# Kernel tuning notes

Hardware: AMD Instinct MI355X
Metric: run time of the kernel (lower is better)

Reference implementation:

```python
import jax, jax.numpy as jnp
import numpy as np
from jax import lax

D, H, HD, DEPTH = 200, 10, 20, 12   # embed_dim, heads, head_dim, depth
NCH, A = 64, 8                       # EEG channels x time windows -> 512 patches (+cls)
NUM_REL = (2 * NCH - 1) * (2 * A - 1) + 3  # 1908


def make_rel_index(wh, ww):
    # exact port of the torch relative_position_index construction
    coords = np.stack(np.meshgrid(np.arange(wh), np.arange(ww), indexing='ij')).reshape(2, -1)
    rel = (coords[:, :, None] - coords[:, None, :]).transpose(1, 2, 0)
    rel[..., 0] += wh - 1
    rel[..., 1] += ww - 1
    rel[..., 0] *= 2 * ww - 1
    n = wh * ww + 1
    num_rel = (2 * wh - 1) * (2 * ww - 1) + 3
    idx = np.zeros((n, n), dtype=np.int32)
    idx[1:, 1:] = rel.sum(-1)
    idx[0, :] = num_rel - 3
    idx[:, 0] = num_rel - 2
    idx[0, 0] = num_rel - 1
    return idx


def gelu(x):
    return jax.nn.gelu(x, approximate=False)


def layer_norm(x, g, b, eps=1e-6):
    m = x.mean(-1, keepdims=True)
    v = ((x - m) ** 2).mean(-1, keepdims=True)
    return (x - m) * lax.rsqrt(v + eps) * g + b


def group_norm(x, g, b, groups=4, eps=1e-5):
    B, C, Hh, W = x.shape
    xr = x.reshape(B, groups, C // groups, Hh, W)
    m = xr.mean((2, 3, 4), keepdims=True)
    v = ((xr - m) ** 2).mean((2, 3, 4), keepdims=True)
    xr = ((xr - m) * lax.rsqrt(v + eps)).reshape(B, C, Hh, W)
    return xr * g[None, :, None, None] + b[None, :, None, None]


def conv2d(x, w, b, stride, pad):
    y = lax.conv_general_dilated(x, w, window_strides=stride, padding=pad,
                                 dimension_numbers=('NCHW', 'OIHW', 'NCHW'))
    return y + b[None, :, None, None]


def setup_inputs() -> dict:
    B = 8
    key = jax.random.key(0)
    ks = iter(jax.random.split(key, 40))
    rn = lambda shape, s=0.02: jax.random.normal(next(ks), shape, dtype=jnp.float32) * s
    z = lambda shape: jnp.zeros(shape, jnp.float32)
    o = lambda shape: jnp.ones(shape, jnp.float32)
    inp = {}
    inp['x'] = jax.random.normal(next(ks), (B, NCH, A, 200), dtype=jnp.float32)
    inp['conv1_w'] = rn((8, 1, 1, 15), 0.1); inp['conv1_b'] = z(8)
    inp['gn1_g'] = o(8); inp['gn1_b'] = z(8)
    inp['conv2_w'] = rn((8, 8, 1, 3), 0.1); inp['conv2_b'] = z(8)
    inp['gn2_g'] = o(8); inp['gn2_b'] = z(8)
    inp['conv3_w'] = rn((8, 8, 1, 3), 0.1); inp['conv3_b'] = z(8)
    inp['gn3_g'] = o(8); inp['gn3_b'] = z(8)
    inp['cls_token'] = rn((1, 1, D)); inp['pos_embed'] = rn((1, NCH + 1, D))
    inp['time_embed'] = rn((1, 16, D))
    inp['ln1_g'] = o((DEPTH, D)); inp['ln1_b'] = z((DEPTH, D))
    inp['qkv_w'] = rn((DEPTH, 3 * D, D))
    inp['rel_bias_table'] = rn((DEPTH, NUM_REL, H))
    inp['proj_w'] = rn((DEPTH, D, D)); inp['proj_b'] = z((DEPTH, D))
    inp['gamma1'] = 0.1 * o((DEPTH, D))
    inp['ln2_g'] = o((DEPTH, D)); inp['ln2_b'] = z((DEPTH, D))
    inp['fc1_w'] = rn((DEPTH, 4 * D, D)); inp['fc1_b'] = z((DEPTH, 4 * D))
    inp['fc2_w'] = rn((DEPTH, D, 4 * D)); inp['fc2_b'] = z((DEPTH, D))
    inp['gamma2'] = 0.1 * o((DEPTH, D))
    inp['fc_norm_g'] = o(D); inp['fc_norm_b'] = z(D)
    inp['head_w'] = rn((4, D)); inp['head_b'] = z(4)
    inp['rel_pos_index'] = jnp.asarray(make_rel_index(NCH, A))
    return inp


def reference(x, conv1_w, conv1_b, gn1_g, gn1_b, conv2_w, conv2_b, gn2_g, gn2_b,
              conv3_w, conv3_b, gn3_g, gn3_b, cls_token, pos_embed, time_embed,
              ln1_g, ln1_b, qkv_w, rel_bias_table, proj_w, proj_b, gamma1,
              ln2_g, ln2_b, fc1_w, fc1_b, fc2_w, fc2_b, gamma2,
              fc_norm_g, fc_norm_b, head_w, head_b, rel_pos_index):
    B = x.shape[0]
    # TemporalConv patch embed: (B, NCH, A, 200) -> (B, NCH*A, D)
    h = x.reshape(B, 1, NCH * A, -1)
    h = gelu(group_norm(conv2d(h, conv1_w, conv1_b, (1, 8), [(0, 0), (7, 7)]), gn1_g, gn1_b))
    h = gelu(group_norm(conv2d(h, conv2_w, conv2_b, (1, 1), [(0, 0), (1, 1)]), gn2_g, gn2_b))
    h = gelu(group_norm(conv2d(h, conv3_w, conv3_b, (1, 1), [(0, 0), (1, 1)]), gn3_g, gn3_b))
    h = h.transpose(0, 2, 3, 1).reshape(B, NCH * A, D)  # 'B C NA T -> B NA (T C)'
    # cls token + per-electrode pos embed + temporal embed
    h = jnp.concatenate([jnp.broadcast_to(cls_token, (B, 1, D)), h], axis=1)
    pos_p = jnp.repeat(pos_embed[:, 1:, None, :], A, axis=2).reshape(1, NCH * A, D)
    h = h + jnp.concatenate([pos_embed[:, :1], pos_p], axis=1)
    te = jnp.broadcast_to(time_embed[:, None, :A, :], (1, NCH, A, D)).reshape(1, NCH * A, D)
    h = jnp.concatenate([h[:, :1], h[:, 1:] + te], axis=1)
    N = h.shape[1]  # 513
    scale = HD ** -0.5
    for d in range(DEPTH):
        y = layer_norm(h, ln1_g[d], ln1_b[d])
        qkv = (y @ qkv_w[d].T).reshape(B, N, 3, H, HD).transpose(2, 0, 3, 1, 4)
        q, k, v = qkv[0], qkv[1], qkv[2]
        attn = jnp.einsum('bhnd,bhmd->bhnm', q * scale, k)
        attn = attn + rel_bias_table[d][rel_pos_index].transpose(2, 0, 1)[None]
        attn = jax.nn.softmax(attn, axis=-1)
        o = jnp.einsum('bhnm,bhmd->bhnd', attn, v)
        o = o.transpose(0, 2, 1, 3).reshape(B, N, D) @ proj_w[d].T + proj_b[d]
        h = h + gamma1[d] * o
        y = layer_norm(h, ln2_g[d], ln2_b[d])
        y = gelu(y @ fc1_w[d].T + fc1_b[d]) @ fc2_w[d].T + fc2_b[d]
        h = h + gamma2[d] * y
    pooled = layer_norm(h[:, 1:].mean(1), fc_norm_g, fc_norm_b)  # use_mean_pooling
    return pooled @ head_w.T + head_b
```

## Files before the change

kernel.cpp:

```cpp
#include <hip/hip_runtime.h>
#include <math.h>

#define DEV static __device__ __forceinline__

typedef __attribute__((ext_vector_type(8))) short bf16x8;
typedef __attribute__((ext_vector_type(4))) float f32x4;

DEV float gelu_exact(float x) {
    return 0.5f * x * (1.0f + erff(x * 0.70710678118654752f));
}

DEV short f2bf(float f) {
    union { float f; unsigned u; } v; v.f = f;
    unsigned r = v.u + 0x7FFF + ((v.u >> 16) & 1);
    return (short)(r >> 16);
}

DEV float bf2f(unsigned short b) {
    union { unsigned u; float f; } v; v.u = ((unsigned)b) << 16;
    return v.f;
}

DEV unsigned pack2bf(float a, float b) {
    return ((unsigned)(unsigned short)f2bf(a)) | (((unsigned)(unsigned short)f2bf(b)) << 16);
}

DEV void gload_lds16(const void* g, void* lds) {
    __builtin_amdgcn_global_load_lds(
        (const __attribute__((address_space(1))) void*)g,
        (__attribute__((address_space(3))) void*)lds, 16, 0, 0);
}

__global__ void conv1_kernel(const float* __restrict__ x, const float* __restrict__ w,
                             const float* __restrict__ bias, float* __restrict__ out) {
    int idx = blockIdx.x * blockDim.x + threadIdx.x;
    const int total = 8 * 8 * 512 * 25;
    if (idx >= total) return;
    int ow = idx % 25;
    int p  = (idx / 25) % 512;
    int oc = (idx / (25 * 512)) % 8;
    int b  = idx / (25 * 512 * 8);
    const float* xp = x + b * 512 * 200 + p * 200;
    const float* wp = w + oc * 15;
    float acc = bias[oc];
    int t0 = ow * 8 - 7;
#pragma unroll
    for (int k = 0; k < 15; k++) {
        int t = t0 + k;
        if (t >= 0 && t < 200) acc += wp[k] * xp[t];
    }
    out[idx] = acc;
}

__global__ void conv3x1_kernel(const float* __restrict__ in, const float* __restrict__ w,
                               const float* __restrict__ bias, float* __restrict__ out) {
    int idx = blockIdx.x * blockDim.x + threadIdx.x;
    const int total = 8 * 8 * 512 * 25;
    if (idx >= total) return;
    int ow = idx % 25;
    int p  = (idx / 25) % 512;
    int oc = (idx / 12800) & 7;
    int b  = idx / 102400;
    float acc = bias[oc];
#pragma unroll
    for (int ic = 0; ic < 8; ic++) {
        const float* ip = in + b * 102400 + ic * 12800 + p * 25;
        const float* wp = w + oc * 24 + ic * 3;
        if (ow > 0)  acc += wp[0] * ip[ow - 1];
        acc += wp[1] * ip[ow];
        if (ow < 24) acc += wp[2] * ip[ow + 1];
    }
    out[idx] = acc;
}

__global__ void gn_stats_kernel(const float* __restrict__ buf, float* __restrict__ stats) {
    int b = blockIdx.x >> 2, g = blockIdx.x & 3;
    const float* base = buf + b * 102400 + g * 2 * 12800;
    float s = 0.f, s2 = 0.f;
    for (int l = threadIdx.x; l < 25600; l += 256) {
        float v = base[l];
        s += v; s2 += v * v;
    }
    __shared__ float ss[256], ss2[256];
    ss[threadIdx.x] = s; ss2[threadIdx.x] = s2;
    __syncthreads();
    for (int o = 128; o; o >>= 1) {
        if (threadIdx.x < o) { ss[threadIdx.x] += ss[threadIdx.x + o]; ss2[threadIdx.x] += ss2[threadIdx.x + o]; }
        __syncthreads();
    }
    if (threadIdx.x == 0) {
        float m = ss[0] / 25600.f;
        float v = ss2[0] / 25600.f - m * m;
        stats[blockIdx.x * 2] = m;
        stats[blockIdx.x * 2 + 1] = v;
    }
}

__global__ void gn_apply_kernel(float* __restrict__ buf, const float* __restrict__ stats,
                                const float* __restrict__ g, const float* __restrict__ bb) {
    int idx = blockIdx.x * blockDim.x + threadIdx.x;
    if (idx >= 8 * 102400) return;
    int c = (idx / 12800) & 7;
    int b = idx / 102400;
    int grp = c >> 1;
    float m = stats[(b * 4 + grp) * 2];
    float v = stats[(b * 4 + grp) * 2 + 1];
    float val = (buf[idx] - m) * rsqrtf(v + 1e-5f) * g[c] + bb[c];
    buf[idx] = gelu_exact(val);
}

__global__ void embed_kernel(const float* __restrict__ conv, const float* __restrict__ cls,
                             const float* __restrict__ pos, const float* __restrict__ te,
                             float* __restrict__ h) {
    int idx = blockIdx.x * blockDim.x + threadIdx.x;
    if (idx >= 8 * 513 * 200) return;
    int d = idx % 200;
    int n = (idx / 200) % 513;
    int b = idx / (200 * 513);
    float val;
    if (n == 0) {
        val = cls[d] + pos[d];
    } else {
        int p = n - 1;
        int t = d >> 3;
        int c = d & 7;
        val = conv[b * 102400 + c * 12800 + p * 25 + t];
        int ch = p >> 3, tw = p & 7;
        val += pos[(1 + ch) * 200 + d] + te[tw * 200 + d];
    }
    h[idx] = val;
}

__global__ void convpad_kernel(const float* __restrict__ src, short* __restrict__ dst,
                               int R, int K, int KP) {
    int idx = blockIdx.x * blockDim.x + threadIdx.x;
    if (idx >= R * KP) return;
    int r = idx / KP, c = idx % KP;
    dst[idx] = (c < K) ? f2bf(src[r * K + c]) : (short)0;
}

__global__ __launch_bounds__(256) void bias_lds_kernel(const float* __restrict__ table,
                                                       const int* __restrict__ ridx,
                                                       short* __restrict__ bias) {
    __shared__ float tl[1908];
    const int qt = blockIdx.x, hh = blockIdx.y, d = blockIdx.z;
    const float* tab = table + d * 19080;
    for (int i = threadIdx.x; i < 1908; i += 256) tl[i] = tab[i * 10 + hh];
    __syncthreads();
    const int q0 = qt * 64;
    const int nrows = min(64, 513 - q0);
    short* obase = bias + ((size_t)d * 10 + hh) * 513 * 576;
#pragma unroll 2
    for (int lin = threadIdx.x; lin < nrows * 144; lin += 256) {
        int r = lin / 144, j = lin % 144;
        int q = q0 + r;
        const int* rp = ridx + q * 513;
        int k0 = j * 4;
        float v[4];
#pragma unroll
        for (int e = 0; e < 4; e++) {
            int k = k0 + e;
            v[e] = (k < 513) ? tl[rp[k]] : 0.f;
        }
        uint2 pk;
        pk.x = pack2bf(v[0], v[1]);
        pk.y = pack2bf(v[2], v[3]);
        *(uint2*)&obase[(size_t)q * 576 + k0] = pk;
    }
}

__global__ __launch_bounds__(256) void ln_kernel(const float* __restrict__ in,
                                                 const float* __restrict__ g,
                                                 const float* __restrict__ b,
                                                 short* __restrict__ out) {
    int row = blockIdx.x * 4 + (threadIdx.x >> 6);
    int lane = threadIdx.x & 63;
    const float* x = in + (size_t)row * 200;
    float v[4];
    float s = 0.f;
#pragma unroll
    for (int i = 0; i < 4; i++) {
        int d = lane + i * 64;
        v[i] = (d < 200) ? x[d] : 0.f;
        s += v[i];
    }
#pragma unroll
    for (int o = 32; o; o >>= 1) s += __shfl_xor(s, o);
    float mean = s * (1.f / 200.f);
    float s2 = 0.f;
#pragma unroll
    for (int i = 0; i < 4; i++) {
        int d = lane + i * 64;
        float dv = (d < 200) ? (v[i] - mean) : 0.f;
        s2 += dv * dv;
    }
#pragma unroll
    for (int o = 32; o; o >>= 1) s2 += __shfl_xor(s2, o);
    float rstd = rsqrtf(s2 * (1.f / 200.f) + 1e-6f);
#pragma unroll
    for (int i = 0; i < 4; i++) {
        int d = lane + i * 64;
        float val = (d < 200) ? (v[i] - mean) * rstd * g[d] + b[d] : 0.f;
        out[(size_t)row * 256 + d] = f2bf(val);
    }
}

template <int EPI, int BM, int BN>
__global__ __launch_bounds__(256) void gemm_bf(const short* __restrict__ A,
                                               const short* __restrict__ W,
                                               float* __restrict__ Cf,
                                               short* __restrict__ Cb,
                                               const float* __restrict__ res,
                                               const float* __restrict__ bias,
                                               const float* __restrict__ gamma,
                                               int M, int N, int KP, int ldc, int NPout,
                                               short* __restrict__ Qb = nullptr,
                                               short* __restrict__ Kb = nullptr,
                                               short* __restrict__ Vt = nullptr) {
    constexpr int WM = BM / 2, WN = BN / 2;
    constexpr int AM = WM / 16, BNr = WN / 16;
    constexpr int LOADS = (BM + BN) / 32;
    __shared__ __align__(16) short Ss[2][(BM + BN) * 64];

    const int tid = threadIdx.x;
    const int w = tid >> 6, l = tid & 63;
    const int wm = (w >> 1) * WM, wn = (w & 1) * WN;
    const int bm = blockIdx.y * BM, bn = blockIdx.x * BN;

    f32x4 acc[AM][BNr] = {};

    auto stage = [&](int buf, int k0) {
#pragma unroll
        for (int it = 0; it < LOADS; it++) {
            int lin = it * 256 + tid;
            int row = lin >> 3, slot = lin & 7;
            int srcslot = slot ^ (row & 7);
            const short* g;
            if (it * 32 < BM) {
                g = A + (size_t)(bm + row) * KP + k0 + srcslot * 8;
            } else {
                g = W + (size_t)(bn + row - BM) * KP + k0 + srcslot * 8;
            }
            gload_lds16(g, (char*)Ss[buf] + lin * 16);
        }
    };

    const int nk = KP >> 6;
    stage(0, 0);
    int cur = 0;
    for (int kstep = 0; kstep < nk; kstep++) {
        if (kstep + 1 < nk) {
            stage(cur ^ 1, (kstep + 1) << 6);
            if constexpr (LOADS == 6) asm volatile("s_waitcnt vmcnt(6)" ::: "memory");
            else                      asm volatile("s_waitcnt vmcnt(4)" ::: "memory");
        } else {
            asm volatile("s_waitcnt vmcnt(0)" ::: "memory");
        }
        __builtin_amdgcn_s_barrier();

        const char* Sc = (const char*)Ss[cur];
#pragma unroll
        for (int kk = 0; kk < 2; kk++) {
            const int kbyte = kk * 64 + (l >> 4) * 16;
            bf16x8 af[AM], bfr[BNr];
#pragma unroll
            for (int i = 0; i < AM; i++) {
                int r = wm + i * 16 + (l & 15);
                af[i] = *(const bf16x8*)(Sc + r * 128 + (kbyte ^ ((r & 7) << 4)));
            }
#pragma unroll
            for (int j = 0; j < BNr; j++) {
                int r = BM + wn + j * 16 + (l & 15);
                bfr[j] = *(const bf16x8*)(Sc + r * 128 + (kbyte ^ ((r & 7) << 4)));
            }
#pragma unroll
            for (int i = 0; i < AM; i++)
#pragma unroll
                for (int j = 0; j < BNr; j++)
                    acc[i][j] = __builtin_amdgcn_mfma_f32_16x16x32_bf16(af[i], bfr[j], acc[i][j], 0, 0, 0);
        }
        __builtin_amdgcn_s_barrier();
        cur ^= 1;
    }

    const int col0 = bn + wn + (l & 15);
    const int rbase = (l >> 4) * 4;
#pragma unroll
    for (int i = 0; i < AM; i++) {
#pragma unroll
        for (int r = 0; r < 4; r++) {
            int gm = bm + wm + i * 16 + rbase + r;
            if (gm >= M) continue;
#pragma unroll
            for (int j = 0; j < BNr; j++) {
                int gn = col0 + j * 16;
                float v = acc[i][j][r];
                if (EPI == 0) {
                    if (gn < N) Cf[(size_t)gm * ldc + gn] = v;
                } else if (EPI == 1) {
                    if (gn < N) Cf[(size_t)gm * ldc + gn] =
                        res[(size_t)gm * ldc + gn] + gamma[gn] * (v + bias[gn]);
                } else if (EPI == 2) {
                    if (gn < NPout)
                        Cb[(size_t)gm * ldc + gn] = (gn < N) ? f2bf(gelu_exact(v + bias[gn])) : (short)0;
                } else {
                    if (gn < 600) {
                        int bb2 = gm / 513, n = gm - bb2 * 513;
                        if (gn < 200) {
                            int hq = gn / 20, dq = gn - hq * 20;
                            Qb[((size_t)(bb2 * 10 + hq) * 576 + n) * 32 + dq] =
                                f2bf(v * 0.22360679774997896f);
                        } else if (gn < 400) {
                            int gk = gn - 200, hk = gk / 20, dk = gk - hk * 20;
                            Kb[((size_t)(bb2 * 10 + hk) * 576 + n) * 32 + dk] = f2bf(v);
                        } else {
                            int gv = gn - 400, hv = gv / 20, dv2 = gv - hv * 20;
                            Vt[((size_t)(bb2 * 10 + hv) * 32 + dv2) * 576 + n] = f2bf(v);
                        }
                    }
                }
            }
        }
    }
}

__global__ __launch_bounds__(256) void attn_mfma2(const short* __restrict__ Qb,
                                                  const short* __restrict__ Kb,
                                                  const short* __restrict__ Vt,
                                                  const short* __restrict__ biasb,
                                                  short* __restrict__ ob) {
    __shared__ __align__(16) short Klds[2][64 * 32];
    __shared__ __align__(16) short Vlds[2][32 * 64];
    __shared__ __align__(16) short Blds[2][64 * 64];
    __shared__ __align__(16) short Pl[4 * 16 * 72];

    const int orig = blockIdx.x;
    const int wg = (orig & 7) * 90 + (orig >> 3);
    const int hh = wg / 72;
    const int rem = wg % 72;
    const int qt = rem >> 3, b = rem & 7;

    const int t = threadIdx.x, wave = t >> 6, l = t & 63;
    const int lq = l & 15, hi = l >> 4;
    const int n = qt * 64 + wave * 16 + lq;
    const int nc = min(n, 512);

    const size_t bh = (size_t)(b * 10 + hh);
    const short* Kbase = Kb + bh * 576 * 32;
    const short* Vbase = Vt + bh * 32 * 576;
    const short* Bbase = biasb + (size_t)hh * 513 * 576;

    bf16x8 qf = *(const bf16x8*)&Qb[(bh * 576 + nc) * 32 + hi * 8];

    const int krow = t >> 2, kch = t & 3;
    const short* ksrc = Kbase + (size_t)krow * 32 + (kch ^ ((krow >> 2) & 3)) * 8;
    const int vrow = t >> 3, vch = t & 7;
    const short* vsrc = Vbase + (size_t)vrow * 576 + (vch ^ (vrow & 7)) * 8;
    const int b0row = t >> 3, b0ch = t & 7;
    const short* bsrc0 = Bbase + (size_t)min(qt * 64 + b0row, 512) * 576 + (b0ch ^ (b0row & 7)) * 8;
    const int b1row = 32 + (t >> 3);
    const short* bsrc1 = Bbase + (size_t)min(qt * 64 + b1row, 512) * 576 + (b0ch ^ (b1row & 7)) * 8;

    float mrun = -1e30f, lsum = 0.f;
    f32x4 oacc0 = {}, oacc1 = {};
    const f32x4 zero4 = {};

    gload_lds16(ksrc, (char*)Klds[0] + t * 16);
    gload_lds16(vsrc, (char*)Vlds[0] + t * 16);
    gload_lds16(bsrc0, (char*)Blds[0] + t * 16);
    gload_lds16(bsrc1, (char*)Blds[0] + 4096 + t * 16);

    int cur = 0;
    for (int kt = 0; kt < 9; kt++) {
        const int koff = kt * 64;
        if (kt < 8) {
            const int knext = koff + 64;
            gload_lds16(ksrc + (size_t)knext * 32, (char*)Klds[cur ^ 1] + t * 16);
            gload_lds16(vsrc + knext, (char*)Vlds[cur ^ 1] + t * 16);
            gload_lds16(bsrc0 + knext, (char*)Blds[cur ^ 1] + t * 16);
            gload_lds16(bsrc1 + knext, (char*)Blds[cur ^ 1] + 4096 + t * 16);
            asm volatile("s_waitcnt vmcnt(4)" ::: "memory");
        } else {
            asm volatile("s_waitcnt vmcnt(0)" ::: "memory");
        }
        __builtin_amdgcn_s_barrier();

        const short* Kc = Klds[cur];
        const short* Vc = Vlds[cur];
        const short* Bc = Blds[cur];

        f32x4 s[4];
        __builtin_amdgcn_s_setprio(1);
#pragma unroll
        for (int c = 0; c < 4; c++) {
            int r = c * 16 + lq;
            bf16x8 kf = *(const bf16x8*)((const char*)Kc + r * 64 + ((hi ^ ((lq >> 2) & 3)) << 4));
            s[c] = __builtin_amdgcn_mfma_f32_16x16x32_bf16(kf, qf, zero4, 0, 0, 0);
        }
        __builtin_amdgcn_s_setprio(0);

        const int brow = wave * 16 + lq;
        float sv[4][4];
        float tm = -1e30f;
#pragma unroll
        for (int c = 0; c < 4; c++) {
            uint2 bl = *(const uint2*)((const char*)Bc + brow * 128 +
                                       (((2 * c + (hi >> 1)) ^ (lq & 7)) << 4) + (hi & 1) * 8);
            float bv[4] = { bf2f((unsigned short)(bl.x & 0xFFFF)), bf2f((unsigned short)(bl.x >> 16)),
                            bf2f((unsigned short)(bl.y & 0xFFFF)), bf2f((unsigned short)(bl.y >> 16)) };
            int kglob = koff + c * 16 + hi * 4;
#pragma unroll
            for (int r = 0; r < 4; r++) {
                float val = s[c][r] + bv[r];
                if (kglob + r > 512) val = -1e30f;
                sv[c][r] = val;
                tm = fmaxf(tm, val);
            }
        }
        tm = fmaxf(tm, __shfl_xor(tm, 16));
        tm = fmaxf(tm, __shfl_xor(tm, 32));
        float mnew = fmaxf(mrun, tm);
        float resc = __expf(mrun - mnew);
        mrun = mnew;

        float ts = 0.f;
#pragma unroll
        for (int c = 0; c < 4; c++) {
            float p0 = __expf(sv[c][0] - mnew);
            float p1 = __expf(sv[c][1] - mnew);
            float p2 = __expf(sv[c][2] - mnew);
            float p3 = __expf(sv[c][3] - mnew);
            ts += (p0 + p1) + (p2 + p3);
            uint2 pk;
            pk.x = pack2bf(p0, p1);
            pk.y = pack2bf(p2, p3);
            *(uint2*)&Pl[wave * 1152 + lq * 72 + c * 16 + hi * 4] = pk;
        }
        ts += __shfl_xor(ts, 16);
        ts += __shfl_xor(ts, 32);
        lsum = lsum * resc + ts;
        oacc0 *= resc;
        oacc1 *= resc;

        __builtin_amdgcn_s_setprio(1);
#pragma unroll
        for (int kc = 0; kc < 2; kc++) {
            bf16x8 pf = *(const bf16x8*)&Pl[wave * 1152 + lq * 72 + kc * 32 + hi * 8];
            bf16x8 vf0 = *(const bf16x8*)((const char*)Vc + lq * 128 +
                                          (((kc * 4 + hi) ^ (lq & 7)) << 4));
            bf16x8 vf1 = *(const bf16x8*)((const char*)Vc + (16 + lq) * 128 +
                                          (((kc * 4 + hi) ^ (lq & 7)) << 4));
            oacc0 = __builtin_amdgcn_mfma_f32_16x16x32_bf16(vf0, pf, oacc0, 0, 0, 0);
            oacc1 = __builtin_amdgcn_mfma_f32_16x16x32_bf16(vf1, pf, oacc1, 0, 0, 0);
        }
        __builtin_amdgcn_s_setprio(0);

        __builtin_amdgcn_s_barrier();
        cur ^= 1;
    }

    if (n < 513) {
        float inv = 1.f / lsum;
        short* op = ob + (size_t)(b * 513 + n) * 256 + hh * 20;
        {
            uint2 pk;
            pk.x = pack2bf(oacc0[0] * inv, oacc0[1] * inv);
            pk.y = pack2bf(oacc0[2] * inv, oacc0[3] * inv);
            *(uint2*)&op[hi * 4] = pk;
        }
        if (hi == 0) {
            uint2 pk;
            pk.x = pack2bf(oacc1[0] * inv, oacc1[1] * inv);
            pk.y = pack2bf(oacc1[2] * inv, oacc1[3] * inv);
            *(uint2*)&op[16] = pk;
        }
    }
}

__global__ __launch_bounds__(256) void final_kernel(const float* __restrict__ h,
                                                    const float* __restrict__ g,
                                                    const float* __restrict__ bb,
                                                    const float* __restrict__ hw,
                                                    const float* __restrict__ hb,
                                                    float* __restrict__ out) {
    __shared__ float pool[256];
    __shared__ float red[256];
    int b = blockIdx.x, t = threadIdx.x;
    float s = 0.f;
    if (t < 200) {
        const float* hp = h + b * 513 * 200 + 200 + t;
        for (int p = 0; p < 512; p++) s += hp[p * 200];
        s *= (1.f / 512.f);
    }
    pool[t] = (t < 200) ? s : 0.f;
    red[t] = pool[t];
    __syncthreads();
    for (int o = 128; o; o >>= 1) {
        if (t < o) red[t] += red[t + o];
        __syncthreads();
    }
    float mean = red[0] / 200.f;
    __syncthreads();
    float dv = (t < 200) ? (pool[t] - mean) : 0.f;
    red[t] = dv * dv;
    __syncthreads();
    for (int o = 128; o; o >>= 1) {
        if (t < o) red[t] += red[t + o];
        __syncthreads();
    }
    float var = red[0] / 200.f;
    float rstd = rsqrtf(var + 1e-6f);
    __syncthreads();
    if (t < 200) pool[t] = (pool[t] - mean) * rstd * g[t] + bb[t];
    __syncthreads();
    if (t < 4) {
        float acc = hb[t];
        for (int d2 = 0; d2 < 200; d2++) acc += pool[d2] * hw[t * 200 + d2];
        out[b * 4 + t] = acc;
    }
}

extern "C" void kernel_launch(void* const* d_in, const int* in_sizes, int n_in,
                              void* d_out, int out_size, void* d_ws, size_t ws_size,
                              hipStream_t stream) {
    const float* x        = (const float*)d_in[0];
    const float* conv1_w  = (const float*)d_in[1];
    const float* conv1_b  = (const float*)d_in[2];
    const float* gn1_g    = (const float*)d_in[3];
    const float* gn1_b    = (const float*)d_in[4];
    const float* conv2_w  = (const float*)d_in[5];
    const float* conv2_b  = (const float*)d_in[6];
    const float* gn2_g    = (const float*)d_in[7];
    const float* gn2_b    = (const float*)d_in[8];
    const float* conv3_w  = (const float*)d_in[9];
    const float* conv3_b  = (const float*)d_in[10];
    const float* gn3_g    = (const float*)d_in[11];
    const float* gn3_b    = (const float*)d_in[12];
    const float* cls_tok  = (const float*)d_in[13];
    const float* pos_emb  = (const float*)d_in[14];
    const float* time_emb = (const float*)d_in[15];
    const float* ln1_g    = (const float*)d_in[16];
    const float* ln1_b    = (const float*)d_in[17];
    const float* qkv_w    = (const float*)d_in[18];
    const float* rel_tab  = (const float*)d_in[19];
    const float* proj_w   = (const float*)d_in[20];
    const float* proj_b   = (const float*)d_in[21];
    const float* gamma1   = (const float*)d_in[22];
    const float* ln2_g    = (const float*)d_in[23];
    const float* ln2_b    = (const float*)d_in[24];
    const float* fc1_w    = (const float*)d_in[25];
    const float* fc1_b    = (const float*)d_in[26];
    const float* fc2_w    = (const float*)d_in[27];
    const float* fc2_b    = (const float*)d_in[28];
    const float* gamma2   = (const float*)d_in[29];
    const float* fcn_g    = (const float*)d_in[30];
    const float* fcn_b    = (const float*)d_in[31];
    const float* head_w   = (const float*)d_in[32];
    const float* head_b   = (const float*)d_in[33];
    const int*   rel_idx  = (const int*)d_in[34];

    char* p = (char*)d_ws;
    float* h    = (float*)p; p += 3283200;
    char* qreg = p;
    float* c1   = (float*)qreg;
    float* c2   = c1 + 819200;
    short* Qb   = (short*)qreg;
    short* Kb   = Qb + 1474560;
    short* Vt   = Kb + 1474560;
    short* mlp  = (short*)qreg;
    p += 9849600;
    short* y    = (short*)p; p += 2101248;
    short* ob   = (short*)p; p += 2101248;
    short* wqkv = (short*)p; p += 3686400;
    short* wproj= (short*)p; p += 1228800;
    short* wfc1 = (short*)p; p += 4915200;
    short* wfc2 = (short*)p; p += 3993600;
    short* biasb= (short*)p; p += 12 * 5909760;
    float* stats= (float*)p;

    convpad_kernel<<<(7200 * 256 + 255) / 256, 256, 0, stream>>>(qkv_w, wqkv, 7200, 200, 256);
    convpad_kernel<<<(2400 * 256 + 255) / 256, 256, 0, stream>>>(proj_w, wproj, 2400, 200, 256);
    convpad_kernel<<<(9600 * 256 + 255) / 256, 256, 0, stream>>>(fc1_w, wfc1, 9600, 200, 256);
    convpad_kernel<<<(2400 * 832 + 255) / 256, 256, 0, stream>>>(fc2_w, wfc2, 2400, 800, 832);
    bias_lds_kernel<<<dim3(9, 10, 12), 256, 0, stream>>>(rel_tab, rel_idx, biasb);
    hipMemsetAsync(ob, 0, 2101248, stream);

    conv1_kernel<<<3200, 256, 0, stream>>>(x, conv1_w, conv1_b, c1);
    gn_stats_kernel<<<32, 256, 0, stream>>>(c1, stats);
    gn_apply_kernel<<<3200, 256, 0, stream>>>(c1, stats, gn1_g, gn1_b);
    conv3x1_kernel<<<3200, 256, 0, stream>>>(c1, conv2_w, conv2_b, c2);
    gn_stats_kernel<<<32, 256, 0, stream>>>(c2, stats);
    gn_apply_kernel<<<3200, 256, 0, stream>>>(c2, stats, gn2_g, gn2_b);
    conv3x1_kernel<<<3200, 256, 0, stream>>>(c2, conv3_w, conv3_b, c1);
    gn_stats_kernel<<<32, 256, 0, stream>>>(c1, stats);
    gn_apply_kernel<<<3200, 256, 0, stream>>>(c1, stats, gn3_g, gn3_b);
    embed_kernel<<<(820800 + 255) / 256, 256, 0, stream>>>(c1, cls_tok, pos_emb, time_emb, h);

    hipMemsetAsync(Qb, 0, 3 * 1474560 * 2, stream);

    for (int d = 0; d < 12; d++) {
        ln_kernel<<<1026, 256, 0, stream>>>(h, ln1_g + d * 200, ln1_b + d * 200, y);
        gemm_bf<3, 64, 128><<<dim3(5, 65), 256, 0, stream>>>(y, wqkv + d * 153600,
                                                             nullptr, nullptr, nullptr, nullptr, nullptr,
                                                             4104, 600, 256, 0, 0, Qb, Kb, Vt);
        attn_mfma2<<<720, 256, 0, stream>>>(Qb, Kb, Vt, biasb + (size_t)d * 2954880, ob);
        gemm_bf<1, 64, 64><<<dim3(4, 65), 256, 0, stream>>>(ob, wproj + d * 51200, h, nullptr,
                                                            h, proj_b + d * 200, gamma1 + d * 200,
                                                            4104, 200, 256, 200, 0);
        ln_kernel<<<1026, 256, 0, stream>>>(h, ln2_g + d * 200, ln2_b + d * 200, y);
        gemm_bf<2, 64, 128><<<dim3(7, 65), 256, 0, stream>>>(y, wfc1 + d * 204800, nullptr, mlp,
                                                             nullptr, fc1_b + d * 800, nullptr,
                                                             4104, 800, 256, 832, 832);
        gemm_bf<1, 64, 64><<<dim3(4, 65), 256, 0, stream>>>(mlp, wfc2 + d * 166400, h, nullptr,
                                                            h, fc2_b + d * 200, gamma2 + d * 200,
                                                            4104, 200, 832, 200, 0);
    }

    final_kernel<<<8, 256, 0, stream>>>(h, fcn_g, fcn_b, head_w, head_b, (float*)d_out);
}
```

Before: 1.092 ms.

## Load attention bias directly to registers, shrink GEMM tiles, vectorize weight conversion

The attention kernel stops staging the relative-position bias tile through double-buffered LDS. Each lane now reads its own bias values straight from global memory into registers, which removes the bias async copies and frees LDS. The QKV and FC1 GEMMs switch from 64x128 to 64x64 tiles with more blocks, to raise parallelism on the many-CU device. The weight padding/conversion kernel now processes four elements per thread with float4 loads. The direct bias loads are less coalesced and sit on the critical path before the softmax, and the smaller GEMM tiles reduce reuse.

```diff
diff --git a/kernel.cpp b/kernel.cpp
--- a/kernel.cpp
+++ b/kernel.cpp
@@ -134,9 +134,21 @@
 __global__ void convpad_kernel(const float* __restrict__ src, short* __restrict__ dst,
                                int R, int K, int KP) {
     int idx = blockIdx.x * blockDim.x + threadIdx.x;
-    if (idx >= R * KP) return;
-    int r = idx / KP, c = idx % KP;
-    dst[idx] = (c < K) ? f2bf(src[r * K + c]) : (short)0;
+    int total = R * (KP >> 2);
+    if (idx >= total) return;
+    int r = idx / (KP >> 2);
+    int c4 = (idx - r * (KP >> 2)) << 2;
+    short4 o;
+    if (c4 + 3 < K) {
+        float4 f = *(const float4*)&src[(size_t)r * K + c4];
+        o.x = f2bf(f.x); o.y = f2bf(f.y); o.z = f2bf(f.z); o.w = f2bf(f.w);
+    } else {
+        o.x = (c4 + 0 < K) ? f2bf(src[(size_t)r * K + c4 + 0]) : (short)0;
+        o.y = (c4 + 1 < K) ? f2bf(src[(size_t)r * K + c4 + 1]) : (short)0;
+        o.z = (c4 + 2 < K) ? f2bf(src[(size_t)r * K + c4 + 2]) : (short)0;
+        o.w = (c4 + 3 < K) ? f2bf(src[(size_t)r * K + c4 + 3]) : (short)0;
+    }
+    *(short4*)&dst[(size_t)r * KP + c4] = o;
 }
 
 __global__ __launch_bounds__(256) void bias_lds_kernel(const float* __restrict__ table,
@@ -331,7 +343,6 @@
                                                   short* __restrict__ ob) {
     __shared__ __align__(16) short Klds[2][64 * 32];
     __shared__ __align__(16) short Vlds[2][32 * 64];
-    __shared__ __align__(16) short Blds[2][64 * 64];
     __shared__ __align__(16) short Pl[4 * 16 * 72];
 
     const int orig = blockIdx.x;
@@ -348,7 +359,7 @@
     const size_t bh = (size_t)(b * 10 + hh);
     const short* Kbase = Kb + bh * 576 * 32;
     const short* Vbase = Vt + bh * 32 * 576;
-    const short* Bbase = biasb + (size_t)hh * 513 * 576;
+    const short* Brow  = biasb + ((size_t)hh * 513 + nc) * 576;
 
     bf16x8 qf = *(const bf16x8*)&Qb[(bh * 576 + nc) * 32 + hi * 8];
 
@@ -356,10 +367,6 @@
     const short* ksrc = Kbase + (size_t)krow * 32 + (kch ^ ((krow >> 2) & 3)) * 8;
     const int vrow = t >> 3, vch = t & 7;
     const short* vsrc = Vbase + (size_t)vrow * 576 + (vch ^ (vrow & 7)) * 8;
-    const int b0row = t >> 3, b0ch = t & 7;
-    const short* bsrc0 = Bbase + (size_t)min(qt * 64 + b0row, 512) * 576 + (b0ch ^ (b0row & 7)) * 8;
-    const int b1row = 32 + (t >> 3);
-    const short* bsrc1 = Bbase + (size_t)min(qt * 64 + b1row, 512) * 576 + (b0ch ^ (b1row & 7)) * 8;
 
     float mrun = -1e30f, lsum = 0.f;
     f32x4 oacc0 = {}, oacc1 = {};
@@ -367,19 +374,21 @@
 
     gload_lds16(ksrc, (char*)Klds[0] + t * 16);
     gload_lds16(vsrc, (char*)Vlds[0] + t * 16);
-    gload_lds16(bsrc0, (char*)Blds[0] + t * 16);
-    gload_lds16(bsrc1, (char*)Blds[0] + 4096 + t * 16);
 
     int cur = 0;
     for (int kt = 0; kt < 9; kt++) {
         const int koff = kt * 64;
+
+        uint2 bl[4];
+#pragma unroll
+        for (int c = 0; c < 4; c++)
+            bl[c] = *(const uint2*)&Brow[koff + c * 16 + hi * 4];
+
         if (kt < 8) {
             const int knext = koff + 64;
             gload_lds16(ksrc + (size_t)knext * 32, (char*)Klds[cur ^ 1] + t * 16);
             gload_lds16(vsrc + knext, (char*)Vlds[cur ^ 1] + t * 16);
-            gload_lds16(bsrc0 + knext, (char*)Blds[cur ^ 1] + t * 16);
-            gload_lds16(bsrc1 + knext, (char*)Blds[cur ^ 1] + 4096 + t * 16);
-            asm volatile("s_waitcnt vmcnt(4)" ::: "memory");
+            asm volatile("s_waitcnt vmcnt(2)" ::: "memory");
         } else {
             asm volatile("s_waitcnt vmcnt(0)" ::: "memory");
         }
@@ -387,7 +396,6 @@
 
         const short* Kc = Klds[cur];
         const short* Vc = Vlds[cur];
-        const short* Bc = Blds[cur];
 
         f32x4 s[4];
         __builtin_amdgcn_s_setprio(1);
@@ -399,15 +407,12 @@
         }
         __builtin_amdgcn_s_setprio(0);
 
-        const int brow = wave * 16 + lq;
         float sv[4][4];
         float tm = -1e30f;
 #pragma unroll
         for (int c = 0; c < 4; c++) {
-            uint2 bl = *(const uint2*)((const char*)Bc + brow * 128 +
-                                       (((2 * c + (hi >> 1)) ^ (lq & 7)) << 4) + (hi & 1) * 8);
-            float bv[4] = { bf2f((unsigned short)(bl.x & 0xFFFF)), bf2f((unsigned short)(bl.x >> 16)),
-                            bf2f((unsigned short)(bl.y & 0xFFFF)), bf2f((unsigned short)(bl.y >> 16)) };
+            float bv[4] = { bf2f((unsigned short)(bl[c].x & 0xFFFF)), bf2f((unsigned short)(bl[c].x >> 16)),
+                            bf2f((unsigned short)(bl[c].y & 0xFFFF)), bf2f((unsigned short)(bl[c].y >> 16)) };
             int kglob = koff + c * 16 + hi * 4;
 #pragma unroll
             for (int r = 0; r < 4; r++) {
@@ -578,10 +583,10 @@
     short* biasb= (short*)p; p += 12 * 5909760;
     float* stats= (float*)p;
 
-    convpad_kernel<<<(7200 * 256 + 255) / 256, 256, 0, stream>>>(qkv_w, wqkv, 7200, 200, 256);
-    convpad_kernel<<<(2400 * 256 + 255) / 256, 256, 0, stream>>>(proj_w, wproj, 2400, 200, 256);
-    convpad_kernel<<<(9600 * 256 + 255) / 256, 256, 0, stream>>>(fc1_w, wfc1, 9600, 200, 256);
-    convpad_kernel<<<(2400 * 832 + 255) / 256, 256, 0, stream>>>(fc2_w, wfc2, 2400, 800, 832);
+    convpad_kernel<<<(7200 * 64 + 255) / 256, 256, 0, stream>>>(qkv_w, wqkv, 7200, 200, 256);
+    convpad_kernel<<<(2400 * 64 + 255) / 256, 256, 0, stream>>>(proj_w, wproj, 2400, 200, 256);
+    convpad_kernel<<<(9600 * 64 + 255) / 256, 256, 0, stream>>>(fc1_w, wfc1, 9600, 200, 256);
+    convpad_kernel<<<(2400 * 208 + 255) / 256, 256, 0, stream>>>(fc2_w, wfc2, 2400, 800, 832);
     bias_lds_kernel<<<dim3(9, 10, 12), 256, 0, stream>>>(rel_tab, rel_idx, biasb);
     hipMemsetAsync(ob, 0, 2101248, stream);
 
@@ -600,7 +605,7 @@
 
     for (int d = 0; d < 12; d++) {
         ln_kernel<<<1026, 256, 0, stream>>>(h, ln1_g + d * 200, ln1_b + d * 200, y);
-        gemm_bf<3, 64, 128><<<dim3(5, 65), 256, 0, stream>>>(y, wqkv + d * 153600,
+        gemm_bf<3, 64, 64><<<dim3(10, 65), 256, 0, stream>>>(y, wqkv + d * 153600,
                                                              nullptr, nullptr, nullptr, nullptr, nullptr,
                                                              4104, 600, 256, 0, 0, Qb, Kb, Vt);
         attn_mfma2<<<720, 256, 0, stream>>>(Qb, Kb, Vt, biasb + (size_t)d * 2954880, ob);
@@ -608,7 +613,7 @@
                                                             h, proj_b + d * 200, gamma1 + d * 200,
                                                             4104, 200, 256, 200, 0);
         ln_kernel<<<1026, 256, 0, stream>>>(h, ln2_g + d * 200, ln2_b + d * 200, y);
-        gemm_bf<2, 64, 128><<<dim3(7, 65), 256, 0, stream>>>(y, wfc1 + d * 204800, nullptr, mlp,
+        gemm_bf<2, 64, 64><<<dim3(13, 65), 256, 0, stream>>>(y, wfc1 + d * 204800, nullptr, mlp,
                                                              nullptr, fc1_b + d * 800, nullptr,
                                                              4104, 800, 256, 832, 832);
         gemm_bf<1, 64, 64><<<dim3(4, 65), 256, 0, stream>>>(mlp, wfc2 + d * 166400, h, nullptr,
```

Result: faster. 1.043 ms (-4.5%).
